# Optimization experiments

Measured on AMD Instinct MI355X. Metric: run time of the kernel, lower is better.

The kernel has to match this reference:

```python
import jax, jax.numpy as jnp
import numpy as np

B, L, F = 16, 1080, 2
D = 128          # d_model
NC = 64          # num_cnn_channels
DIN = 256        # expand * d_model
N = 16           # d_state
K = 4            # d_conv
R = 8            # dt_rank = ceil(d_model/16)
OUT = 3
NB = 3           # num_mamba_blocks


def setup_inputs() -> dict:
    key = jax.random.key(0)
    ks = jax.random.split(key, 24)
    nrm = lambda k, shape, s=0.05: (jax.random.normal(k, shape) * s).astype(jnp.float32)
    bn = lambda c: jnp.stack([jnp.ones(c), jnp.zeros(c), jnp.zeros(c), jnp.ones(c)]).astype(jnp.float32)
    return {
        'x': jax.random.normal(ks[0], (B, L, F), dtype=jnp.float32),
        'emb_W': nrm(ks[1], (F, D), 0.5), 'emb_b': jnp.zeros(D, jnp.float32),
        'c3_W': nrm(ks[2], (NC, D, 3)), 'c3_b': jnp.zeros(NC, jnp.float32), 'bn3': bn(NC),
        'c5_W': nrm(ks[3], (NC, D, 5)), 'c5_b': jnp.zeros(NC, jnp.float32), 'bn5': bn(NC),
        'c7_W': nrm(ks[4], (NC, D, 7)), 'c7_b': jnp.zeros(NC, jnp.float32), 'bn7': bn(NC),
        'cf_W': nrm(ks[5], (D, 3 * NC, 1)), 'cf_b': jnp.zeros(D, jnp.float32), 'bnf': bn(D),
        'ln_g': jnp.ones((NB, D), jnp.float32), 'ln_b': jnp.zeros((NB, D), jnp.float32),
        'in_W': nrm(ks[6], (NB, 2 * DIN, D)),
        'mconv_W': nrm(ks[7], (NB, DIN, K), 0.2), 'mconv_b': jnp.zeros((NB, DIN), jnp.float32),
        'xproj_W': nrm(ks[8], (NB, R + 2 * N, DIN)),
        'dt_W': nrm(ks[9], (NB, DIN, R), 0.1), 'dt_b': jnp.full((NB, DIN), -1.0, jnp.float32),
        'A_log': jnp.tile(jnp.log(jnp.arange(1.0, N + 1.0, dtype=jnp.float32)), (NB, DIN, 1)),
        'Dp': jnp.ones((NB, DIN), jnp.float32),
        'out_W': nrm(ks[10], (NB, D, DIN)),
        'flin_W': nrm(ks[11], (D, 2 * D)), 'flin_b': jnp.zeros(D, jnp.float32),
        'fc_W': nrm(ks[12], (OUT, D)), 'fc_b': jnp.zeros(OUT, jnp.float32),
    }


def conv1d(x, W, b, pad):
    # x: (B,C,L), W: (O,C,K)
    y = jax.lax.conv_general_dilated(x, W, (1,), [(pad, pad)],
                                     dimension_numbers=('NCH', 'OIH', 'NCH'))
    return y + b[None, :, None]


def bn_relu(x, bn, eps=1e-5):
    g, b, m, v = bn  # each (C,)
    return jax.nn.relu((x - m[None, :, None]) * (g / jnp.sqrt(v + eps))[None, :, None] + b[None, :, None])


def layernorm(x, g, b, eps=1e-5):
    mu = x.mean(-1, keepdims=True)
    var = ((x - mu) ** 2).mean(-1, keepdims=True)
    return (x - mu) / jnp.sqrt(var + eps) * g + b


def pos_encoding(seq_len, d_model):
    pos = jnp.arange(seq_len, dtype=jnp.float32)[:, None]
    div = jnp.exp(jnp.arange(0, d_model, 2, dtype=jnp.float32) * (-np.log(10000.0) / d_model))
    pe = jnp.zeros((seq_len, d_model), jnp.float32)
    pe = pe.at[:, 0::2].set(jnp.sin(pos * div)).at[:, 1::2].set(jnp.cos(pos * div))
    return pe


def selective_scan(u, dt, A, Bm, Cm, Dp):
    # u,dt: (b,l,d); A: (d,n); Bm,Cm: (b,l,n); Dp: (d,)
    dA = jnp.exp(dt[..., None] * A)                    # (b,l,d,n)
    dBu = (dt * u)[..., None] * Bm[:, :, None, :]      # (b,l,d,n)

    def step(h, t):
        dA_t, dBu_t, C_t = t
        h = dA_t * h + dBu_t                           # (b,d,n)
        return h, jnp.einsum('bdn,bn->bd', h, C_t)

    h0 = jnp.zeros((u.shape[0], u.shape[2], A.shape[1]), u.dtype)
    _, ys = jax.lax.scan(step, h0, (jnp.swapaxes(dA, 0, 1), jnp.swapaxes(dBu, 0, 1), jnp.swapaxes(Cm, 0, 1)))
    return jnp.swapaxes(ys, 0, 1) + u * Dp


def mamba_block(x, in_W, conv_W, conv_b, xproj_W, dt_W, dt_b, A_log, Dp, out_W):
    xz = x @ in_W.T                                    # (b,l,2*din)
    xs, z = jnp.split(xz, 2, axis=-1)
    xc = jnp.swapaxes(xs, 1, 2)                        # (b,din,l)
    xc = jax.lax.conv_general_dilated(xc, conv_W[:, None, :], (1,), [(K - 1, 0)],
                                      dimension_numbers=('NCH', 'OIH', 'NCH'),
                                      feature_group_count=DIN)
    u = jax.nn.silu(jnp.swapaxes(xc + conv_b[None, :, None], 1, 2))  # (b,l,din)
    dbl = u @ xproj_W.T
    dt, Bm, Cm = dbl[..., :R], dbl[..., R:R + N], dbl[..., R + N:]
    dt = jax.nn.softplus(dt @ dt_W.T + dt_b)
    A = -jnp.exp(A_log)
    y = selective_scan(u, dt, A, Bm, Cm, Dp)
    return (y * jax.nn.silu(z)) @ out_W.T


def reference(x, emb_W, emb_b, c3_W, c3_b, bn3, c5_W, c5_b, bn5, c7_W, c7_b, bn7,
              cf_W, cf_b, bnf, ln_g, ln_b, in_W, mconv_W, mconv_b, xproj_W,
              dt_W, dt_b, A_log, Dp, out_W, flin_W, flin_b, fc_W, fc_b):
    xe = x @ emb_W + emb_b + pos_encoding(x.shape[1], emb_W.shape[1])  # (B,L,D)
    ci = jnp.swapaxes(xe, 1, 2)                                        # (B,D,L)
    o3 = bn_relu(conv1d(ci, c3_W, c3_b, 1), bn3)
    o5 = bn_relu(conv1d(ci, c5_W, c5_b, 2), bn5)
    o7 = bn_relu(conv1d(ci, c7_W, c7_b, 3), bn7)
    cc = jnp.concatenate([o3, o5, o7], axis=1)                         # (B,3*NC,L)
    cf = bn_relu(conv1d(cc, cf_W, cf_b, 0), bnf)
    cnn_feat = jnp.swapaxes(cf, 1, 2)                                  # (B,L,D)
    m = xe
    for i in range(NB):  # Sequential(LN, Mamba, Dropout) -- no residual, dropout=eval
        m = mamba_block(layernorm(m, ln_g[i], ln_b[i]), in_W[i], mconv_W[i], mconv_b[i],
                        xproj_W[i], dt_W[i], dt_b[i], A_log[i], Dp[i], out_W[i])
    fused = jax.nn.relu(jnp.concatenate([cnn_feat, m], axis=-1) @ flin_W.T + flin_b)
    pooled = fused.mean(axis=1)                                        # AdaptiveAvgPool1d(1)
    return pooled @ fc_W.T + fc_b
```

## Files before the change

### kernel.cpp

```cpp
#include <hip/hip_runtime.h>
#include <math.h>

#define LSEQ   1080
#define NBATCH 16
#define BLROWS (LSEQ*NBATCH)
#define CHN    27
#define LCH    40

typedef __bf16  bf16x8 __attribute__((ext_vector_type(8)));
typedef float   f32x4  __attribute__((ext_vector_type(4)));
typedef short   short8 __attribute__((ext_vector_type(8)));
typedef short   short4v __attribute__((ext_vector_type(4)));

__device__ __forceinline__ float silu_f(float x) { return x / (1.f + __expf(-x)); }

__device__ __forceinline__ unsigned short f2bf(float f) {
    unsigned int u = __float_as_uint(f);
    u += 0x7fffu + ((u >> 16) & 1u);
    return (unsigned short)(u >> 16);
}
__device__ __forceinline__ float bf2f(unsigned short h) {
    return __uint_as_float(((unsigned int)h) << 16);
}
__device__ __forceinline__ void split_bf(float v, unsigned short& h, unsigned short& l) {
    h = f2bf(v);
    l = f2bf(v - bf2f(h));
}

__global__ __launch_bounds__(256) void embed_kernel(
    const float* __restrict__ x, const float* __restrict__ embW,
    const float* __restrict__ embb, float* __restrict__ xe)
{
    int idx = blockIdx.x * 256 + threadIdx.x;
    if (idx >= BLROWS * 128) return;
    int d = idx & 127;
    int r = idx >> 7;
    int t = r % LSEQ;
    float x0 = x[(size_t)r * 2], x1 = x[(size_t)r * 2 + 1];
    int i2 = d & 126;
    float div = expf((float)i2 * (-9.210340371976184f / 128.f));
    float arg = (float)t * div;
    float pe = (d & 1) ? cosf(arg) : sinf(arg);
    xe[idx] = fmaf(x0, embW[d], fmaf(x1, embW[128 + d], embb[d] + pe));
}

#define JOB_W192  172032
#define JOB_CF    196608
#define JOB_IN    393216
#define JOB_XP    442368
#define JOB_OT    540672
#define JOB_FL    573440
#define JOB_END   574080
__global__ __launch_bounds__(256) void convw_all(
    const float* __restrict__ c3W, const float* __restrict__ c5W,
    const float* __restrict__ c7W, const float* __restrict__ cfW,
    const float* __restrict__ inW, const float* __restrict__ xpW,
    const float* __restrict__ otW, const float* __restrict__ flW,
    const float* __restrict__ c3b, const float* __restrict__ c5b, const float* __restrict__ c7b,
    const float* __restrict__ bn3, const float* __restrict__ bn5, const float* __restrict__ bn7,
    const float* __restrict__ cfb, const float* __restrict__ bnf,
    unsigned short* __restrict__ w192h, unsigned short* __restrict__ w192l,
    unsigned short* __restrict__ cfh, unsigned short* __restrict__ cfl,
    unsigned short* __restrict__ inh, unsigned short* __restrict__ inl,
    unsigned short* __restrict__ xph, unsigned short* __restrict__ xpl,
    unsigned short* __restrict__ oth, unsigned short* __restrict__ otl,
    unsigned short* __restrict__ flh, unsigned short* __restrict__ fll,
    float* __restrict__ schpack)
{
    int idx = blockIdx.x * 256 + threadIdx.x;
    if (idx >= JOB_END) return;
    if (idx >= JOB_FL + 32768) { return; }
    float v;
    unsigned short *dh, *dl;
    int off;
    if (idx < JOB_W192) {
        off = idx;
        int n = off / 896, kk = off % 896;
        int slot = kk >> 7, d = kk & 127;
        int br = n >> 6, c = n & 63;
        int KT = 3 + 2 * br, pad = 1 + br;
        int tp = slot - 3 + pad;
        const float* w = (br == 0) ? c3W : (br == 1) ? c5W : c7W;
        v = (tp >= 0 && tp < KT) ? w[((c << 7) + d) * KT + tp] : 0.f;
        dh = w192h; dl = w192l;
    } else if (idx < JOB_CF) {
        off = idx - JOB_W192; v = cfW[off]; dh = cfh; dl = cfl;
    } else if (idx < JOB_IN) {
        off = idx - JOB_CF; v = inW[off]; dh = inh; dl = inl;
    } else if (idx < JOB_XP) {
        off = idx - JOB_IN;
        int k = off & 255, n = (off >> 8) & 63, blk = off >> 14;
        v = (n < 40) ? xpW[((size_t)blk * 40 + n) * 256 + k] : 0.f;
        dh = xph; dl = xpl;
    } else if (idx < JOB_OT) {
        off = idx - JOB_XP; v = otW[off]; dh = oth; dl = otl;
    } else if (idx < JOB_FL) {
        off = idx - JOB_OT; v = flW[off]; dh = flh; dl = fll;
    } else {
        int j = idx - JOB_FL;
        if (j < 384) {
            int col = (j < 192) ? j : j - 192;
            int isSh = j >= 192;
            int br = col >> 6, c = col & 63;
            const float* bn = (br == 0) ? bn3 : (br == 1) ? bn5 : bn7;
            float bias = ((br == 0) ? c3b : (br == 1) ? c5b : c7b)[c];
            float g = bn[c], bb = bn[64 + c], m = bn[128 + c], vv = bn[192 + c];
            float scale = g * rsqrtf(vv + 1e-5f);
            float shift = (bias - m) * scale + bb;
            schpack[j] = isSh ? shift : scale;
        } else {
            int j2 = j - 384;
            int col = j2 & 127;
            int isSh = j2 >= 128;
            float g = bnf[col], bb = bnf[128 + col], m = bnf[256 + col], vv = bnf[384 + col];
            float scale = g * rsqrtf(vv + 1e-5f);
            float shift = (cfb[col] - m) * scale + bb;
            schpack[384 + j2] = isSh ? shift : scale;
        }
        return;
    }
    unsigned short h, l;
    split_bf(v, h, l);
    dh[off] = h; dl[off] = l;
}

__global__ __launch_bounds__(256) void gemm_conv(
    const float* __restrict__ xe,
    const unsigned short* __restrict__ Wh, const unsigned short* __restrict__ Wl,
    const float* __restrict__ sc, const float* __restrict__ sh,
    unsigned short* __restrict__ Ch, unsigned short* __restrict__ Cl)
{
    __shared__ unsigned short Ah[70][40], Al[70][40];
    __shared__ unsigned short Bh[64][136], Bl[64][136];
    const int tid = threadIdx.x;
    const int n0 = blockIdx.x * 64, t0 = blockIdx.y * 64, b = blockIdx.z;
    const float* Ab = xe + (size_t)b * LSEQ * 128;
    const int lane = tid & 63, wid = tid >> 6;
    const int wr = wid >> 1, wc = wid & 1;
    const int fr = lane & 15, fq = lane >> 4;
    f32x4 acc[2][2];
#pragma unroll
    for (int m = 0; m < 2; ++m)
#pragma unroll
        for (int n = 0; n < 2; ++n) acc[m][n] = (f32x4){0.f, 0.f, 0.f, 0.f};

    for (int ks = 0; ks < 128; ks += 32) {
#pragma unroll
        for (int l = 0; l < 3; ++l) {
            int c = tid + l * 256;
            if (c < 560) {
                int row = c >> 3, kq = (c & 7) << 2;
                int ts = t0 - 3 + row;
                float4 av = make_float4(0.f, 0.f, 0.f, 0.f);
                if (ts >= 0 && ts < LSEQ)
                    av = *(const float4*)(Ab + (size_t)ts * 128 + ks + kq);
                alignas(8) unsigned short hs[4], ls[4];
                float fv[4] = {av.x, av.y, av.z, av.w};
#pragma unroll
                for (int j = 0; j < 4; ++j) split_bf(fv[j], hs[j], ls[j]);
                *(short4v*)&Ah[row][kq] = *(short4v*)hs;
                *(short4v*)&Al[row][kq] = *(short4v*)ls;
            }
        }
        for (int g = 0; g < 2; ++g) {
            const int ntap = (g == 0) ? 4 : 3;
#pragma unroll
            for (int l = 0; l < 4; ++l) {
                int c = tid + l * 256;
                int col = c >> 4, rem = c & 15, tt = rem >> 2, kq = (rem & 3) << 3;
                if (tt < ntap) {
                    int tap = g * 4 + tt;
                    size_t s = (size_t)(n0 + col) * 896 + tap * 128 + ks + kq;
                    *(short8*)&Bh[col][tt * 32 + kq] = *(const short8*)&Wh[s];
                    *(short8*)&Bl[col][tt * 32 + kq] = *(const short8*)&Wl[s];
                }
            }
            __syncthreads();
            for (int tt = 0; tt < ntap; ++tt) {
                int tap = g * 4 + tt;
                bf16x8 bhf[2], blf[2];
#pragma unroll
                for (int n = 0; n < 2; ++n) {
                    int col = wc * 32 + n * 16 + fr;
                    bhf[n] = __builtin_bit_cast(bf16x8, *(const short8*)&Bh[col][tt * 32 + fq * 8]);
                    blf[n] = __builtin_bit_cast(bf16x8, *(const short8*)&Bl[col][tt * 32 + fq * 8]);
                }
#pragma unroll
                for (int m = 0; m < 2; ++m) {
                    int rowA = wr * 32 + m * 16 + fr + tap;
                    bf16x8 ahf = __builtin_bit_cast(bf16x8, *(const short8*)&Ah[rowA][fq * 8]);
                    bf16x8 alf = __builtin_bit_cast(bf16x8, *(const short8*)&Al[rowA][fq * 8]);
#pragma unroll
                    for (int n = 0; n < 2; ++n) {
                        acc[m][n] = __builtin_amdgcn_mfma_f32_16x16x32_bf16(ahf, bhf[n], acc[m][n], 0, 0, 0);
                        acc[m][n] = __builtin_amdgcn_mfma_f32_16x16x32_bf16(ahf, blf[n], acc[m][n], 0, 0, 0);
                        acc[m][n] = __builtin_amdgcn_mfma_f32_16x16x32_bf16(alf, bhf[n], acc[m][n], 0, 0, 0);
                    }
                }
            }
            __syncthreads();
        }
    }
    unsigned short* Chb = Ch + (size_t)b * LSEQ * 192;
    unsigned short* Clb = Cl + (size_t)b * LSEQ * 192;
#pragma unroll
    for (int m = 0; m < 2; ++m) {
#pragma unroll
        for (int n = 0; n < 2; ++n) {
            int colg = n0 + wc * 32 + n * 16 + fr;
            float scl = sc[colg], shf2 = sh[colg];
#pragma unroll
            for (int r = 0; r < 4; ++r) {
                int t = t0 + wr * 32 + m * 16 + fq * 4 + r;
                if (t >= LSEQ) continue;
                float v = fmaf(acc[m][n][r], scl, shf2);
                v = v > 0.f ? v : 0.f;
                unsigned short h, l;
                split_bf(v, h, l);
                Chb[(size_t)t * 192 + colg] = h;
                Clb[(size_t)t * 192 + colg] = l;
            }
        }
    }
}

template<int BM, int BN>
__global__ __launch_bounds__(256) void gemm_plain(
    const unsigned short* __restrict__ Aph, const unsigned short* __restrict__ Apl, int lda,
    const unsigned short* __restrict__ Wh, const unsigned short* __restrict__ Wl, int Kd,
    int Ntot, int epi,
    const float* __restrict__ sc, const float* __restrict__ sh, const float* __restrict__ bias,
    float* __restrict__ Cf, int ldc,
    unsigned short* __restrict__ Ch, unsigned short* __restrict__ Cl, int ldch)
{
    constexpr int WM = BM / 2, WN = BN / 2;
    constexpr int MR = WM / 16, NR = WN / 16;
    constexpr int ACH = (BM * 4) / 256;
    constexpr int BCH = (BN * 4) / 256;
    __shared__ unsigned short Ah[BM][40], Al[BM][40];
    __shared__ unsigned short Bh[BN][40], Bl[BN][40];
    const int tid = threadIdx.x;
    const int b = blockIdx.z, t0 = blockIdx.y * BM, n0 = blockIdx.x * BN;
    const unsigned short* Abh = Aph + (size_t)b * LSEQ * lda;
    const unsigned short* Abl = Apl + (size_t)b * LSEQ * lda;
    const int lane = tid & 63, wid = tid >> 6;
    const int wr = wid >> 1, wc = wid & 1;
    const int fr = lane & 15, fq = lane >> 4;
    f32x4 acc[MR][NR];
#pragma unroll
    for (int m = 0; m < MR; ++m)
#pragma unroll
        for (int n = 0; n < NR; ++n) acc[m][n] = (f32x4){0.f, 0.f, 0.f, 0.f};

    const short8 zz = {0, 0, 0, 0, 0, 0, 0, 0};
    for (int ks = 0; ks < Kd; ks += 32) {
#pragma unroll
        for (int l = 0; l < ACH; ++l) {
            int c = tid + l * 256;
            int row = c >> 2, kc = (c & 3) << 3;
            int t = t0 + row;
            short8 vh = zz, vl = zz;
            if (t < LSEQ) {
                size_t s = (size_t)t * lda + ks + kc;
                vh = *(const short8*)&Abh[s];
                vl = *(const short8*)&Abl[s];
            }
            *(short8*)&Ah[row][kc] = vh;
            *(short8*)&Al[row][kc] = vl;
        }
#pragma unroll
        for (int l = 0; l < BCH; ++l) {
            int c = tid + l * 256;
            int col = c >> 2, kc = (c & 3) << 3;
            size_t s = (size_t)(n0 + col) * Kd + ks + kc;
            *(short8*)&Bh[col][kc] = *(const short8*)&Wh[s];
            *(short8*)&Bl[col][kc] = *(const short8*)&Wl[s];
        }
        __syncthreads();
        bf16x8 bhf[NR], blf[NR];
#pragma unroll
        for (int n = 0; n < NR; ++n) {
            int col = wc * WN + n * 16 + fr;
            bhf[n] = __builtin_bit_cast(bf16x8, *(const short8*)&Bh[col][fq * 8]);
            blf[n] = __builtin_bit_cast(bf16x8, *(const short8*)&Bl[col][fq * 8]);
        }
#pragma unroll
        for (int m = 0; m < MR; ++m) {
            int rowr = wr * WM + m * 16 + fr;
            bf16x8 ahf = __builtin_bit_cast(bf16x8, *(const short8*)&Ah[rowr][fq * 8]);
            bf16x8 alf = __builtin_bit_cast(bf16x8, *(const short8*)&Al[rowr][fq * 8]);
#pragma unroll
            for (int n = 0; n < NR; ++n) {
                acc[m][n] = __builtin_amdgcn_mfma_f32_16x16x32_bf16(ahf, bhf[n], acc[m][n], 0, 0, 0);
                acc[m][n] = __builtin_amdgcn_mfma_f32_16x16x32_bf16(ahf, blf[n], acc[m][n], 0, 0, 0);
                acc[m][n] = __builtin_amdgcn_mfma_f32_16x16x32_bf16(alf, bhf[n], acc[m][n], 0, 0, 0);
            }
        }
        __syncthreads();
    }

    float* Cfb = Cf ? Cf + (size_t)b * LSEQ * ldc : nullptr;
    unsigned short* Chb = Ch ? Ch + (size_t)b * LSEQ * ldch : nullptr;
    unsigned short* Clb = Cl ? Cl + (size_t)b * LSEQ * ldch : nullptr;
#pragma unroll
    for (int m = 0; m < MR; ++m) {
#pragma unroll
        for (int n = 0; n < NR; ++n) {
            int colg = n0 + wc * WN + n * 16 + fr;
            if (colg >= Ntot) continue;
#pragma unroll
            for (int r = 0; r < 4; ++r) {
                int t = t0 + wr * WM + m * 16 + fq * 4 + r;
                if (t >= LSEQ) continue;
                float v = acc[m][n][r];
                if (epi == 0) {
                    Cfb[(size_t)t * ldc + colg] = v;
                } else if (epi == 1) {
                    v = fmaf(v, sc[colg], sh[colg]);
                    v = v > 0.f ? v : 0.f;
                    unsigned short h, l;
                    split_bf(v, h, l);
                    Chb[(size_t)t * ldch + colg] = h;
                    Clb[(size_t)t * ldch + colg] = l;
                } else if (epi == 2) {
                    v += bias[colg];
                    v = v > 0.f ? v : 0.f;
                    Cfb[(size_t)t * ldc + colg] = v;
                } else {
                    unsigned short h, l;
                    split_bf(v, h, l);
                    Chb[(size_t)t * ldch + colg] = h;
                    Clb[(size_t)t * ldch + colg] = l;
                }
            }
        }
    }
}

__global__ __launch_bounds__(256) void ln_kernel(
    const float* __restrict__ in, const float* __restrict__ g,
    const float* __restrict__ b2, unsigned short* __restrict__ oh,
    unsigned short* __restrict__ ol)
{
    int lane = threadIdx.x & 63;
    int wid  = threadIdx.x >> 6;
    int row = blockIdx.x * 4 + wid;
    if (row >= BLROWS) return;
    const float* rp = in + (size_t)row * 128;
    float v0 = rp[lane], v1 = rp[lane + 64];
    float s = v0 + v1;
#pragma unroll
    for (int o2 = 32; o2 > 0; o2 >>= 1) s += __shfl_xor(s, o2, 64);
    float mu = s * (1.f / 128.f);
    float d0 = v0 - mu, d1 = v1 - mu;
    float q = d0 * d0 + d1 * d1;
#pragma unroll
    for (int o2 = 32; o2 > 0; o2 >>= 1) q += __shfl_xor(q, o2, 64);
    float rs = 1.f / sqrtf(q * (1.f / 128.f) + 1e-5f);
    float y0 = d0 * rs * g[lane]      + b2[lane];
    float y1 = d1 * rs * g[lane + 64] + b2[lane + 64];
    unsigned short h, l;
    size_t o = (size_t)row * 128;
    split_bf(y0, h, l); oh[o + lane] = h;      ol[o + lane] = l;
    split_bf(y1, h, l); oh[o + lane + 64] = h; ol[o + lane + 64] = l;
}

__global__ __launch_bounds__(256) void mconv_kernel(
    const float* __restrict__ xz, const float* __restrict__ Wc,
    const float* __restrict__ bc, float* __restrict__ u,
    unsigned short* __restrict__ uh, unsigned short* __restrict__ ul)
{
    int idx = blockIdx.x * 256 + threadIdx.x;
    int c = idx & 255;
    int r = idx >> 8;
    if (r >= BLROWS) return;
    int t = r % LSEQ;
    const float* xs = xz + (size_t)r * 512 + c;
    float acc = bc[c];
    if (t >= 3) acc = fmaf(xs[-3 * 512], Wc[c * 4 + 0], acc);
    if (t >= 2) acc = fmaf(xs[-2 * 512], Wc[c * 4 + 1], acc);
    if (t >= 1) acc = fmaf(xs[-1 * 512], Wc[c * 4 + 2], acc);
    acc = fmaf(xs[0], Wc[c * 4 + 3], acc);
    float uv = silu_f(acc);
    size_t o = (size_t)r * 256 + c;
    u[o] = uv;
    unsigned short h, l;
    split_bf(uv, h, l);
    uh[o] = h; ul[o] = l;
}

__global__ __launch_bounds__(256) void dtk_kernel(
    const float* __restrict__ dbl, const float* __restrict__ dtW,
    const float* __restrict__ dtb, float* __restrict__ dtout)
{
    int idx = blockIdx.x * 256 + threadIdx.x;
    int c = idx & 255;
    int r = idx >> 8;
    if (r >= BLROWS) return;
    const float* dr = dbl + (size_t)r * 40;
    float a = dtb[c];
#pragma unroll
    for (int j = 0; j < 8; ++j) a = fmaf(dr[j], dtW[c * 8 + j], a);
    float sp = (a > 20.f) ? a : log1pf(__expf(a));
    dtout[(size_t)r * 256 + c] = sp;
}

__global__ __launch_bounds__(256) void scan1_kernel(
    const float* __restrict__ dt, const float* __restrict__ u,
    const float* __restrict__ dbl, const float* __restrict__ Alog,
    float* __restrict__ P, float* __restrict__ S)
{
    __shared__ float sdt[20][64], su[20][64], sB[20][16];
    int bid = blockIdx.x;
    int dg = bid & 3;
    int rest = bid >> 2;
    int ch = rest % CHN;
    int b  = rest / CHN;
    int tid = threadIdx.x;
    int ng = tid & 3, di = tid >> 2;
    int d0 = dg * 64, d = d0 + di, n0 = ng * 4;
    float A2[4];
#pragma unroll
    for (int j = 0; j < 4; ++j) A2[j] = -__expf(Alog[d * 16 + n0 + j]);
    float p[4] = {1.f, 1.f, 1.f, 1.f}, s[4] = {0.f, 0.f, 0.f, 0.f};
    int r0 = b * LSEQ + ch * LCH;
    for (int ph = 0; ph < 2; ++ph) {
        int rb = r0 + ph * 20;
#pragma unroll
        for (int l = 0; l < 5; ++l) {
            int j = tid + l * 256;
            int row = j >> 6, dc = j & 63;
            sdt[row][dc] = dt[(size_t)(rb + row) * 256 + d0 + dc];
            su [row][dc] = u [(size_t)(rb + row) * 256 + d0 + dc];
        }
        {
            int j = tid;
            if (j < 320) {
                int row = j >> 4, n = j & 15;
                sB[row][n] = dbl[(size_t)(rb + row) * 40 + 8 + n];
            }
        }
        __syncthreads();
#pragma unroll 4
        for (int qi = 0; qi < 20; ++qi) {
            float dtv = sdt[qi][di];
            float dtu = dtv * su[qi][di];
            float4 Br = *(const float4*)&sB[qi][n0];
            float bv[4] = {Br.x, Br.y, Br.z, Br.w};
#pragma unroll
            for (int j = 0; j < 4; ++j) {
                float a = __expf(dtv * A2[j]);
                p[j] *= a;
                s[j] = fmaf(a, s[j], dtu * bv[j]);
            }
        }
        __syncthreads();
    }
    size_t ob = ((size_t)(b * CHN + ch) * 256 + d) * 16 + n0;
    *(float4*)&P[ob] = make_float4(p[0], p[1], p[2], p[3]);
    *(float4*)&S[ob] = make_float4(s[0], s[1], s[2], s[3]);
}

__global__ __launch_bounds__(256) void scan2_kernel(
    const float* __restrict__ P, const float* __restrict__ S, float* __restrict__ H0)
{
    int idx = blockIdx.x * 256 + threadIdx.x;
    int n = idx & 15;
    int d = (idx >> 4) & 255;
    int b = idx >> 12;
    float h = 0.f;
    for (int ch = 0; ch < CHN; ++ch) {
        size_t o = ((size_t)(b * CHN + ch) * 256 + d) * 16 + n;
        H0[o] = h;
        h = fmaf(P[o], h, S[o]);
    }
}

__global__ __launch_bounds__(256) void scan3_kernel(
    const float* __restrict__ dt, const float* __restrict__ u,
    const float* __restrict__ dbl, const float* __restrict__ Alog,
    const float* __restrict__ H0, const float* __restrict__ Dp,
    const float* __restrict__ xz, unsigned short* __restrict__ gh,
    unsigned short* __restrict__ gl)
{
    __shared__ float sdt[20][64], su[20][64], sz[20][64], sB[20][16], sC[20][16];
    int bid = blockIdx.x;
    int dg = bid & 3;
    int rest = bid >> 2;
    int ch = rest % CHN;
    int b  = rest / CHN;
    int tid = threadIdx.x;
    int ng = tid & 3, di = tid >> 2;
    int d0 = dg * 64, d = d0 + di, n0 = ng * 4;
    float A2[4];
#pragma unroll
    for (int j = 0; j < 4; ++j) A2[j] = -__expf(Alog[d * 16 + n0 + j]);
    size_t ob = ((size_t)(b * CHN + ch) * 256 + d) * 16 + n0;
    float4 h4 = *(const float4*)&H0[ob];
    float h[4] = {h4.x, h4.y, h4.z, h4.w};
    float Dpd = Dp[d];
    int r0 = b * LSEQ + ch * LCH;
    for (int ph = 0; ph < 2; ++ph) {
        int rb = r0 + ph * 20;
#pragma unroll
        for (int l = 0; l < 5; ++l) {
            int j = tid + l * 256;
            int row = j >> 6, dc = j & 63;
            sdt[row][dc] = dt[(size_t)(rb + row) * 256 + d0 + dc];
            su [row][dc] = u [(size_t)(rb + row) * 256 + d0 + dc];
            sz [row][dc] = xz[(size_t)(rb + row) * 512 + 256 + d0 + dc];
        }
        {
            int j = tid;
            if (j < 320) {
                int row = j >> 4, n = j & 15;
                sB[row][n] = dbl[(size_t)(rb + row) * 40 + 8 + n];
                sC[row][n] = dbl[(size_t)(rb + row) * 40 + 24 + n];
            }
        }
        __syncthreads();
        for (int qi = 0; qi < 20; ++qi) {
            float dtv = sdt[qi][di];
            float uv  = su[qi][di];
            float dtu = dtv * uv;
            float4 Br = *(const float4*)&sB[qi][n0];
            float4 Cr = *(const float4*)&sC[qi][n0];
            float bv[4] = {Br.x, Br.y, Br.z, Br.w};
            float cv[4] = {Cr.x, Cr.y, Cr.z, Cr.w};
            float pacc = 0.f;
#pragma unroll
            for (int j = 0; j < 4; ++j) {
                float a = __expf(dtv * A2[j]);
                h[j] = fmaf(a, h[j], dtu * bv[j]);
                pacc = fmaf(h[j], cv[j], pacc);
            }
            float acc = pacc + __shfl_xor(pacc, 1);
            acc += __shfl_xor(acc, 2);
            if (ng == 0) {
                float yv = fmaf(uv, Dpd, acc);
                float gv = yv * silu_f(sz[qi][di]);
                unsigned short hh, ll;
                split_bf(gv, hh, ll);
                size_t r = (size_t)(rb + qi);
                gh[r * 256 + d] = hh;
                gl[r * 256 + d] = ll;
            }
        }
        __syncthreads();
    }
}

__global__ __launch_bounds__(128) void pool1_kernel(
    const float* __restrict__ fused, float* __restrict__ part)
{
    int d = threadIdx.x;
    int blk = blockIdx.x;
    int ch = blk % CHN;
    int b  = blk / CHN;
    int t0 = ch * LCH;
    float s = 0.f;
    for (int q = 0; q < LCH; ++q)
        s += fused[((size_t)(b * LSEQ + t0 + q)) * 128 + d];
    part[(size_t)(b * CHN + ch) * 128 + d] = s;
}

__global__ __launch_bounds__(128) void pool2_kernel(
    const float* __restrict__ part, const float* __restrict__ fcW,
    const float* __restrict__ fcb, float* __restrict__ out)
{
    __shared__ float pl[128];
    int d = threadIdx.x;
    int b = blockIdx.x;
    float s = 0.f;
    for (int ch = 0; ch < CHN; ++ch) s += part[(size_t)(b * CHN + ch) * 128 + d];
    pl[d] = s * (1.f / 1080.f);
    __syncthreads();
    if (d < 3) {
        float a = fcb[d];
        for (int dd = 0; dd < 128; ++dd) a = fmaf(pl[dd], fcW[d * 128 + dd], a);
        out[b * 3 + d] = a;
    }
}

extern "C" void kernel_launch(void* const* d_in, const int* in_sizes, int n_in,
                              void* d_out, int out_size, void* d_ws, size_t ws_size,
                              hipStream_t stream)
{
    const float* x    = (const float*)d_in[0];
    const float* embW = (const float*)d_in[1];
    const float* embb = (const float*)d_in[2];
    const float* c3W  = (const float*)d_in[3];
    const float* c3b  = (const float*)d_in[4];
    const float* bn3  = (const float*)d_in[5];
    const float* c5W  = (const float*)d_in[6];
    const float* c5b  = (const float*)d_in[7];
    const float* bn5  = (const float*)d_in[8];
    const float* c7W  = (const float*)d_in[9];
    const float* c7b  = (const float*)d_in[10];
    const float* bn7  = (const float*)d_in[11];
    const float* cfW  = (const float*)d_in[12];
    const float* cfb  = (const float*)d_in[13];
    const float* bnf  = (const float*)d_in[14];
    const float* lng  = (const float*)d_in[15];
    const float* lnb  = (const float*)d_in[16];
    const float* inW  = (const float*)d_in[17];
    const float* mcW  = (const float*)d_in[18];
    const float* mcb  = (const float*)d_in[19];
    const float* xpW  = (const float*)d_in[20];
    const float* dtW  = (const float*)d_in[21];
    const float* dtbp = (const float*)d_in[22];
    const float* Alog = (const float*)d_in[23];
    const float* Dp   = (const float*)d_in[24];
    const float* outW = (const float*)d_in[25];
    const float* flW  = (const float*)d_in[26];
    const float* flb  = (const float*)d_in[27];
    const float* fcW  = (const float*)d_in[28];
    const float* fcb  = (const float*)d_in[29];

    float* ws = (float*)d_ws;
    size_t off = 0;
    auto alloc = [&](size_t n) { float* p = ws + off; off += n; return p; };
    float* xe   = alloc((size_t)BLROWS * 128);
    float* xz   = alloc((size_t)BLROWS * 512);
    float* ub   = alloc((size_t)BLROWS * 256);
    float* dtt  = alloc((size_t)BLROWS * 256);
    float* dbl  = alloc((size_t)BLROWS * 40);
    float* Pb   = alloc((size_t)NBATCH * CHN * 256 * 16);
    float* Sb   = alloc((size_t)NBATCH * CHN * 256 * 16);
    float* h0b  = alloc((size_t)NBATCH * CHN * 256 * 16);
    float* schpack = alloc(640);
    float* fused = xz;
    float* mtail = xz + (size_t)BLROWS * 384;

    off = (off + 3) & ~(size_t)3;
    unsigned short* us = (unsigned short*)(ws + off);
    size_t uo = 0;
    auto ualloc = [&](size_t n) { unsigned short* p = us + uo; uo += n; return p; };
    unsigned short* cch  = ualloc((size_t)BLROWS * 192);
    unsigned short* ccl  = ualloc((size_t)BLROWS * 192);
    unsigned short* finh = ualloc((size_t)BLROWS * 256);
    unsigned short* finl = ualloc((size_t)BLROWS * 256);
    unsigned short* ubh  = ualloc((size_t)BLROWS * 256);
    unsigned short* ubl  = ualloc((size_t)BLROWS * 256);
    unsigned short* w192h = ualloc((size_t)192 * 896); unsigned short* w192l = ualloc((size_t)192 * 896);
    unsigned short* cfh = ualloc(128 * 192); unsigned short* cfl = ualloc(128 * 192);
    unsigned short* inh = ualloc((size_t)1536 * 128); unsigned short* inl = ualloc((size_t)1536 * 128);
    unsigned short* xph = ualloc((size_t)3 * 64 * 256); unsigned short* xpl = ualloc((size_t)3 * 64 * 256);
    unsigned short* oth = ualloc((size_t)384 * 256); unsigned short* otl = ualloc((size_t)384 * 256);
    unsigned short* flh = ualloc((size_t)128 * 256); unsigned short* fll = ualloc((size_t)128 * 256);
    unsigned short* lnxh = cch;
    unsigned short* lnxl = ccl;
    unsigned short* gbh  = ubh;
    unsigned short* gbl  = ubl;
    (void)ws_size; (void)in_sizes; (void)n_in; (void)out_size;

    convw_all<<<(JOB_END + 255) / 256, 256, 0, stream>>>(
        c3W, c5W, c7W, cfW, inW, xpW, outW, flW,
        c3b, c5b, c7b, bn3, bn5, bn7, cfb, bnf,
        w192h, w192l, cfh, cfl, inh, inl, xph, xpl, oth, otl, flh, fll, schpack);

    embed_kernel<<<(BLROWS * 128) / 256, 256, 0, stream>>>(x, embW, embb, xe);

    dim3 gconv(3, 17, NBATCH);
    gemm_conv<<<gconv, 256, 0, stream>>>(xe, w192h, w192l, schpack, schpack + 192, cch, ccl);
    dim3 g17(1, 17, NBATCH);
    gemm_plain<64, 128><<<g17, 256, 0, stream>>>(
        cch, ccl, 192, cfh, cfl, 192, 128, 1,
        schpack + 384, schpack + 512, nullptr, nullptr, 0, finh, finl, 256);

    const int SCAN_BLKS = NBATCH * CHN * 4;
    for (int i = 0; i < 3; ++i) {
        const float* min_ = (i == 0) ? xe : mtail;

        ln_kernel<<<BLROWS / 4, 256, 0, stream>>>(min_, lng + i * 128, lnb + i * 128, lnxh, lnxl);

        dim3 gin(4, 9, NBATCH);
        gemm_plain<128, 128><<<gin, 256, 0, stream>>>(
            lnxh, lnxl, 128, inh + (size_t)i * 512 * 128, inl + (size_t)i * 512 * 128, 128,
            512, 0, nullptr, nullptr, nullptr, xz, 512, nullptr, nullptr, 0);

        mconv_kernel<<<BLROWS, 256, 0, stream>>>(xz, mcW + i * 256 * 4, mcb + i * 256, ub, ubh, ubl);

        gemm_plain<64, 64><<<g17, 256, 0, stream>>>(
            ubh, ubl, 256, xph + (size_t)i * 64 * 256, xpl + (size_t)i * 64 * 256, 256,
            40, 0, nullptr, nullptr, nullptr, dbl, 40, nullptr, nullptr, 0);

        dtk_kernel<<<BLROWS, 256, 0, stream>>>(dbl, dtW + i * 256 * 8, dtbp + i * 256, dtt);

        scan1_kernel<<<SCAN_BLKS, 256, 0, stream>>>(
            dtt, ub, dbl, Alog + i * 256 * 16, Pb, Sb);
        scan2_kernel<<<(NBATCH * 256 * 16) / 256, 256, 0, stream>>>(Pb, Sb, h0b);
        scan3_kernel<<<SCAN_BLKS, 256, 0, stream>>>(
            dtt, ub, dbl, Alog + i * 256 * 16, h0b, Dp + i * 256, xz, gbh, gbl);

        if (i < 2) {
            gemm_plain<64, 128><<<g17, 256, 0, stream>>>(
                gbh, gbl, 256, oth + (size_t)i * 128 * 256, otl + (size_t)i * 128 * 256, 256,
                128, 0, nullptr, nullptr, nullptr, mtail, 128, nullptr, nullptr, 0);
        } else {
            gemm_plain<64, 128><<<g17, 256, 0, stream>>>(
                gbh, gbl, 256, oth + (size_t)i * 128 * 256, otl + (size_t)i * 128 * 256, 256,
                128, 3, nullptr, nullptr, nullptr, nullptr, 0, finh + 128, finl + 128, 256);
        }
    }

    gemm_plain<64, 128><<<g17, 256, 0, stream>>>(
        finh, finl, 256, flh, fll, 256, 128, 2,
        nullptr, nullptr, flb, fused, 128, nullptr, nullptr, 0);

    pool1_kernel<<<NBATCH * CHN, 128, 0, stream>>>(fused, Pb);
    pool2_kernel<<<NBATCH, 128, 0, stream>>>(Pb, fcW, fcb, (float*)d_out);
}
```

Before: 657.0 us.

## Pre-split embeddings to bf16, load scan chunks whole, coalesce gated output writes

The embedding kernel now also writes the hi/lo bf16 split of xe, so the conv GEMM loads ready-made short8 tiles instead of converting floats per tile. Both scan kernels load the full 40-step chunk into shared memory in one vectorized pass instead of two 20-step phases. scan3 stages the gated outputs in shared memory and writes them out as coalesced vector stores. The in-projection GEMM switches to a 64-row tile for more blocks. Costs are extra global buffers, a larger shared-memory footprint in the scans that may lower occupancy, and all lanes now doing the gate computation.

```diff
diff --git a/kernel.cpp b/kernel.cpp
--- a/kernel.cpp
+++ b/kernel.cpp
@@ -29,7 +29,8 @@
 
 __global__ __launch_bounds__(256) void embed_kernel(
     const float* __restrict__ x, const float* __restrict__ embW,
-    const float* __restrict__ embb, float* __restrict__ xe)
+    const float* __restrict__ embb, float* __restrict__ xe,
+    unsigned short* __restrict__ xeh, unsigned short* __restrict__ xel)
 {
     int idx = blockIdx.x * 256 + threadIdx.x;
     if (idx >= BLROWS * 128) return;
@@ -41,7 +42,11 @@
     float div = expf((float)i2 * (-9.210340371976184f / 128.f));
     float arg = (float)t * div;
     float pe = (d & 1) ? cosf(arg) : sinf(arg);
-    xe[idx] = fmaf(x0, embW[d], fmaf(x1, embW[128 + d], embb[d] + pe));
+    float v = fmaf(x0, embW[d], fmaf(x1, embW[128 + d], embb[d] + pe));
+    xe[idx] = v;
+    unsigned short h, l;
+    split_bf(v, h, l);
+    xeh[idx] = h; xel[idx] = l;
 }
 
 #define JOB_W192  172032
@@ -69,7 +74,6 @@
 {
     int idx = blockIdx.x * 256 + threadIdx.x;
     if (idx >= JOB_END) return;
-    if (idx >= JOB_FL + 32768) { return; }
     float v;
     unsigned short *dh, *dl;
     int off;
@@ -125,7 +129,7 @@
 }
 
 __global__ __launch_bounds__(256) void gemm_conv(
-    const float* __restrict__ xe,
+    const unsigned short* __restrict__ Xh, const unsigned short* __restrict__ Xl,
     const unsigned short* __restrict__ Wh, const unsigned short* __restrict__ Wl,
     const float* __restrict__ sc, const float* __restrict__ sh,
     unsigned short* __restrict__ Ch, unsigned short* __restrict__ Cl)
@@ -134,10 +138,11 @@
     __shared__ unsigned short Bh[64][136], Bl[64][136];
     const int tid = threadIdx.x;
     const int n0 = blockIdx.x * 64, t0 = blockIdx.y * 64, b = blockIdx.z;
-    const float* Ab = xe + (size_t)b * LSEQ * 128;
+    const size_t boff = (size_t)b * LSEQ;
     const int lane = tid & 63, wid = tid >> 6;
     const int wr = wid >> 1, wc = wid & 1;
     const int fr = lane & 15, fq = lane >> 4;
+    const short8 zz = {0, 0, 0, 0, 0, 0, 0, 0};
     f32x4 acc[2][2];
 #pragma unroll
     for (int m = 0; m < 2; ++m)
@@ -146,20 +151,19 @@
 
     for (int ks = 0; ks < 128; ks += 32) {
 #pragma unroll
-        for (int l = 0; l < 3; ++l) {
+        for (int l = 0; l < 2; ++l) {
             int c = tid + l * 256;
-            if (c < 560) {
-                int row = c >> 3, kq = (c & 7) << 2;
+            if (c < 280) {
+                int row = c >> 2, kc = (c & 3) << 3;
                 int ts = t0 - 3 + row;
-                float4 av = make_float4(0.f, 0.f, 0.f, 0.f);
-                if (ts >= 0 && ts < LSEQ)
-                    av = *(const float4*)(Ab + (size_t)ts * 128 + ks + kq);
-                alignas(8) unsigned short hs[4], ls[4];
-                float fv[4] = {av.x, av.y, av.z, av.w};
-#pragma unroll
-                for (int j = 0; j < 4; ++j) split_bf(fv[j], hs[j], ls[j]);
-                *(short4v*)&Ah[row][kq] = *(short4v*)hs;
-                *(short4v*)&Al[row][kq] = *(short4v*)ls;
+                short8 vh = zz, vl = zz;
+                if (ts >= 0 && ts < LSEQ) {
+                    size_t s = (boff + ts) * 128 + ks + kc;
+                    vh = *(const short8*)&Xh[s];
+                    vl = *(const short8*)&Xl[s];
+                }
+                *(short8*)&Ah[row][kc] = vh;
+                *(short8*)&Al[row][kc] = vl;
             }
         }
         for (int g = 0; g < 2; ++g) {
@@ -410,7 +414,7 @@
     const float* __restrict__ dbl, const float* __restrict__ Alog,
     float* __restrict__ P, float* __restrict__ S)
 {
-    __shared__ float sdt[20][64], su[20][64], sB[20][16];
+    __shared__ float sdt[40][64], su[40][64], sB[40][16];
     int bid = blockIdx.x;
     int dg = bid & 3;
     int rest = bid >> 2;
@@ -419,42 +423,38 @@
     int tid = threadIdx.x;
     int ng = tid & 3, di = tid >> 2;
     int d0 = dg * 64, d = d0 + di, n0 = ng * 4;
+    int r0 = b * LSEQ + ch * LCH;
+#pragma unroll
+    for (int l = 0; l < 3; ++l) {
+        int j = tid + l * 256;
+        if (j < 640) {
+            int row = j >> 4, q = (j & 15) << 2;
+            size_t s = (size_t)(r0 + row) * 256 + d0 + q;
+            *(float4*)&sdt[row][q] = *(const float4*)&dt[s];
+            *(float4*)&su [row][q] = *(const float4*)&u [s];
+        }
+    }
+    if (tid < 160) {
+        int row = tid >> 2, q = (tid & 3) << 2;
+        *(float4*)&sB[row][q] = *(const float4*)&dbl[(size_t)(r0 + row) * 40 + 8 + q];
+    }
     float A2[4];
 #pragma unroll
     for (int j = 0; j < 4; ++j) A2[j] = -__expf(Alog[d * 16 + n0 + j]);
     float p[4] = {1.f, 1.f, 1.f, 1.f}, s[4] = {0.f, 0.f, 0.f, 0.f};
-    int r0 = b * LSEQ + ch * LCH;
-    for (int ph = 0; ph < 2; ++ph) {
-        int rb = r0 + ph * 20;
-#pragma unroll
-        for (int l = 0; l < 5; ++l) {
-            int j = tid + l * 256;
-            int row = j >> 6, dc = j & 63;
-            sdt[row][dc] = dt[(size_t)(rb + row) * 256 + d0 + dc];
-            su [row][dc] = u [(size_t)(rb + row) * 256 + d0 + dc];
-        }
-        {
-            int j = tid;
-            if (j < 320) {
-                int row = j >> 4, n = j & 15;
-                sB[row][n] = dbl[(size_t)(rb + row) * 40 + 8 + n];
-            }
-        }
-        __syncthreads();
+    __syncthreads();
 #pragma unroll 4
-        for (int qi = 0; qi < 20; ++qi) {
-            float dtv = sdt[qi][di];
-            float dtu = dtv * su[qi][di];
-            float4 Br = *(const float4*)&sB[qi][n0];
-            float bv[4] = {Br.x, Br.y, Br.z, Br.w};
-#pragma unroll
-            for (int j = 0; j < 4; ++j) {
-                float a = __expf(dtv * A2[j]);
-                p[j] *= a;
-                s[j] = fmaf(a, s[j], dtu * bv[j]);
-            }
-        }
-        __syncthreads();
+    for (int qi = 0; qi < LCH; ++qi) {
+        float dtv = sdt[qi][di];
+        float dtu = dtv * su[qi][di];
+        float4 Br = *(const float4*)&sB[qi][n0];
+        float bv[4] = {Br.x, Br.y, Br.z, Br.w};
+#pragma unroll
+        for (int j = 0; j < 4; ++j) {
+            float a = __expf(dtv * A2[j]);
+            p[j] *= a;
+            s[j] = fmaf(a, s[j], dtu * bv[j]);
+        }
     }
     size_t ob = ((size_t)(b * CHN + ch) * 256 + d) * 16 + n0;
     *(float4*)&P[ob] = make_float4(p[0], p[1], p[2], p[3]);
@@ -483,7 +483,7 @@
     const float* __restrict__ xz, unsigned short* __restrict__ gh,
     unsigned short* __restrict__ gl)
 {
-    __shared__ float sdt[20][64], su[20][64], sz[20][64], sB[20][16], sC[20][16];
+    __shared__ float sdt[40][64], su[40][64], sz[40][64], sB[40][16], sC[40][16];
     int bid = blockIdx.x;
     int dg = bid & 3;
     int rest = bid >> 2;
@@ -492,6 +492,23 @@
     int tid = threadIdx.x;
     int ng = tid & 3, di = tid >> 2;
     int d0 = dg * 64, d = d0 + di, n0 = ng * 4;
+    int r0 = b * LSEQ + ch * LCH;
+#pragma unroll
+    for (int l = 0; l < 3; ++l) {
+        int j = tid + l * 256;
+        if (j < 640) {
+            int row = j >> 4, q = (j & 15) << 2;
+            size_t s = (size_t)(r0 + row) * 256 + d0 + q;
+            *(float4*)&sdt[row][q] = *(const float4*)&dt[s];
+            *(float4*)&su [row][q] = *(const float4*)&u [s];
+            *(float4*)&sz [row][q] = *(const float4*)&xz[(size_t)(r0 + row) * 512 + 256 + d0 + q];
+        }
+    }
+    if (tid < 160) {
+        int row = tid >> 2, q = (tid & 3) << 2;
+        *(float4*)&sB[row][q] = *(const float4*)&dbl[(size_t)(r0 + row) * 40 + 8 + q];
+        *(float4*)&sC[row][q] = *(const float4*)&dbl[(size_t)(r0 + row) * 40 + 24 + q];
+    }
     float A2[4];
 #pragma unroll
     for (int j = 0; j < 4; ++j) A2[j] = -__expf(Alog[d * 16 + n0 + j]);
@@ -499,54 +516,43 @@
     float4 h4 = *(const float4*)&H0[ob];
     float h[4] = {h4.x, h4.y, h4.z, h4.w};
     float Dpd = Dp[d];
-    int r0 = b * LSEQ + ch * LCH;
-    for (int ph = 0; ph < 2; ++ph) {
-        int rb = r0 + ph * 20;
-#pragma unroll
-        for (int l = 0; l < 5; ++l) {
-            int j = tid + l * 256;
-            int row = j >> 6, dc = j & 63;
-            sdt[row][dc] = dt[(size_t)(rb + row) * 256 + d0 + dc];
-            su [row][dc] = u [(size_t)(rb + row) * 256 + d0 + dc];
-            sz [row][dc] = xz[(size_t)(rb + row) * 512 + 256 + d0 + dc];
-        }
-        {
-            int j = tid;
-            if (j < 320) {
-                int row = j >> 4, n = j & 15;
-                sB[row][n] = dbl[(size_t)(rb + row) * 40 + 8 + n];
-                sC[row][n] = dbl[(size_t)(rb + row) * 40 + 24 + n];
-            }
-        }
-        __syncthreads();
-        for (int qi = 0; qi < 20; ++qi) {
-            float dtv = sdt[qi][di];
-            float uv  = su[qi][di];
-            float dtu = dtv * uv;
-            float4 Br = *(const float4*)&sB[qi][n0];
-            float4 Cr = *(const float4*)&sC[qi][n0];
-            float bv[4] = {Br.x, Br.y, Br.z, Br.w};
-            float cv[4] = {Cr.x, Cr.y, Cr.z, Cr.w};
-            float pacc = 0.f;
-#pragma unroll
-            for (int j = 0; j < 4; ++j) {
-                float a = __expf(dtv * A2[j]);
-                h[j] = fmaf(a, h[j], dtu * bv[j]);
-                pacc = fmaf(h[j], cv[j], pacc);
-            }
-            float acc = pacc + __shfl_xor(pacc, 1);
-            acc += __shfl_xor(acc, 2);
-            if (ng == 0) {
-                float yv = fmaf(uv, Dpd, acc);
-                float gv = yv * silu_f(sz[qi][di]);
-                unsigned short hh, ll;
-                split_bf(gv, hh, ll);
-                size_t r = (size_t)(rb + qi);
-                gh[r * 256 + d] = hh;
-                gl[r * 256 + d] = ll;
-            }
-        }
-        __syncthreads();
+    __syncthreads();
+    for (int qi = 0; qi < LCH; ++qi) {
+        float dtv = sdt[qi][di];
+        float uv  = su[qi][di];
+        float dtu = dtv * uv;
+        float4 Br = *(const float4*)&sB[qi][n0];
+        float4 Cr = *(const float4*)&sC[qi][n0];
+        float bv[4] = {Br.x, Br.y, Br.z, Br.w};
+        float cv[4] = {Cr.x, Cr.y, Cr.z, Cr.w};
+        float pacc = 0.f;
+#pragma unroll
+        for (int j = 0; j < 4; ++j) {
+            float a = __expf(dtv * A2[j]);
+            h[j] = fmaf(a, h[j], dtu * bv[j]);
+            pacc = fmaf(h[j], cv[j], pacc);
+        }
+        float acc = pacc + __shfl_xor(pacc, 1);
+        acc += __shfl_xor(acc, 2);
+        float yv = fmaf(uv, Dpd, acc);
+        float gv = yv * silu_f(sz[qi][di]);
+        if (ng == 0) sz[qi][di] = gv;
+    }
+    __syncthreads();
+#pragma unroll
+    for (int l = 0; l < 3; ++l) {
+        int j = tid + l * 256;
+        if (j < 640) {
+            int row = j >> 4, q = (j & 15) << 2;
+            float4 gv4 = *(const float4*)&sz[row][q];
+            float gv[4] = {gv4.x, gv4.y, gv4.z, gv4.w};
+            alignas(8) unsigned short hs[4], ls[4];
+#pragma unroll
+            for (int jj = 0; jj < 4; ++jj) split_bf(gv[jj], hs[jj], ls[jj]);
+            size_t o = (size_t)(r0 + row) * 256 + d0 + q;
+            *(short4v*)&gh[o] = *(short4v*)hs;
+            *(short4v*)&gl[o] = *(short4v*)ls;
+        }
     }
 }
 
@@ -642,6 +648,8 @@
     unsigned short* finl = ualloc((size_t)BLROWS * 256);
     unsigned short* ubh  = ualloc((size_t)BLROWS * 256);
     unsigned short* ubl  = ualloc((size_t)BLROWS * 256);
+    unsigned short* xeh  = ualloc((size_t)BLROWS * 128);
+    unsigned short* xel  = ualloc((size_t)BLROWS * 128);
     unsigned short* w192h = ualloc((size_t)192 * 896); unsigned short* w192l = ualloc((size_t)192 * 896);
     unsigned short* cfh = ualloc(128 * 192); unsigned short* cfl = ualloc(128 * 192);
     unsigned short* inh = ualloc((size_t)1536 * 128); unsigned short* inl = ualloc((size_t)1536 * 128);
@@ -659,10 +667,10 @@
         c3b, c5b, c7b, bn3, bn5, bn7, cfb, bnf,
         w192h, w192l, cfh, cfl, inh, inl, xph, xpl, oth, otl, flh, fll, schpack);
 
-    embed_kernel<<<(BLROWS * 128) / 256, 256, 0, stream>>>(x, embW, embb, xe);
+    embed_kernel<<<(BLROWS * 128) / 256, 256, 0, stream>>>(x, embW, embb, xe, xeh, xel);
 
     dim3 gconv(3, 17, NBATCH);
-    gemm_conv<<<gconv, 256, 0, stream>>>(xe, w192h, w192l, schpack, schpack + 192, cch, ccl);
+    gemm_conv<<<gconv, 256, 0, stream>>>(xeh, xel, w192h, w192l, schpack, schpack + 192, cch, ccl);
     dim3 g17(1, 17, NBATCH);
     gemm_plain<64, 128><<<g17, 256, 0, stream>>>(
         cch, ccl, 192, cfh, cfl, 192, 128, 1,
@@ -674,8 +682,8 @@
 
         ln_kernel<<<BLROWS / 4, 256, 0, stream>>>(min_, lng + i * 128, lnb + i * 128, lnxh, lnxl);
 
-        dim3 gin(4, 9, NBATCH);
-        gemm_plain<128, 128><<<gin, 256, 0, stream>>>(
+        dim3 gin(4, 17, NBATCH);
+        gemm_plain<64, 128><<<gin, 256, 0, stream>>>(
             lnxh, lnxl, 128, inh + (size_t)i * 512 * 128, inl + (size_t)i * 512 * 128, 128,
             512, 0, nullptr, nullptr, nullptr, xz, 512, nullptr, nullptr, 0);
 
```

After: 648.6 us. No clear change (-1.3%).
